# Kernel optimization log

Measured on AMD Instinct MI355X. Metric: run time of the kernel, lower is better.

The kernel has to match this reference:

```python
import jax, jax.numpy as jnp
import numpy as np

N_QUBITS = 8
BATCH = 65536
PI = float(np.pi)


def rz_mat(t):
    # diag(e^{-i t/2}, e^{+i t/2}); t scalar or [B]
    t = jnp.asarray(t, jnp.float32).astype(jnp.complex64)
    e = jnp.exp(-0.5j * t)
    z = jnp.zeros_like(e)
    return jnp.stack([jnp.stack([e, z], -1), jnp.stack([z, jnp.conj(e)], -1)], -2)


def ry_mat(t):
    t = jnp.asarray(t, jnp.float32)
    c = jnp.cos(0.5 * t).astype(jnp.complex64)
    s = jnp.sin(0.5 * t).astype(jnp.complex64)
    return jnp.stack([jnp.stack([c, -s], -1), jnp.stack([s, c], -1)], -2)


def u3_mat(t, p, l):
    t = jnp.asarray(t, jnp.float32)
    c = jnp.cos(0.5 * t).astype(jnp.complex64)
    s = jnp.sin(0.5 * t).astype(jnp.complex64)
    ep = jnp.exp(1j * jnp.asarray(p, jnp.float32).astype(jnp.complex64))
    el = jnp.exp(1j * jnp.asarray(l, jnp.float32).astype(jnp.complex64))
    return jnp.stack([jnp.stack([c, -el * s], -1), jnp.stack([ep * s, ep * el * c], -1)], -2)


def apply_1q(state, U, w):
    # state: [B] + [2]*N_QUBITS; wire w is axis w+1 (wire 0 most significant, tq convention)
    s = jnp.moveaxis(state, w + 1, -1)
    if U.ndim == 3:  # batched gate (state prep with per-sample angles)
        s = jnp.einsum('b...i,bji->b...j', s, U)
    else:
        s = jnp.einsum('...i,ji->...j', s, U)
    return jnp.moveaxis(s, -1, w + 1)


def apply_cnot(state, c, t):
    s = jnp.moveaxis(state, (c + 1, t + 1), (-2, -1))
    s = jnp.concatenate([s[..., :1, :], s[..., 1:, ::-1]], axis=-2)
    return jnp.moveaxis(s, (-2, -1), (c + 1, t + 1))


def expval_z(state, w):
    p = jnp.square(jnp.abs(state))
    p = jnp.moveaxis(p, w + 1, 1).reshape(p.shape[0], 2, -1).sum(-1)
    return p[:, 0] - p[:, 1]


def build_state(x):
    # circuit_builder substitute: RY(theta), RZ(phi) on every qubit from |0...0>
    B = x.shape[0]
    theta, phi = x[:, 0], x[:, 1]
    state = jnp.zeros((B, 2 ** N_QUBITS), jnp.complex64).at[:, 0].set(1.0)
    state = state.reshape((B,) + (2,) * N_QUBITS)
    Ry, Rz = ry_mat(theta), rz_mat(phi)  # [B,2,2]
    for w in range(N_QUBITS):
        state = apply_1q(state, Ry, w)
        state = apply_1q(state, Rz, w)
    return state


def block(state, a, b, rzp, ry1p, ry2p, fin=None):
    # ZNOTY two-qubit convolution unitary on wires (a, b)
    fin = b if fin is None else fin
    state = apply_1q(state, rz_mat(-PI / 2), a)
    state = apply_cnot(state, a, b)
    state = apply_1q(state, rz_mat(rzp), b)
    state = apply_1q(state, ry_mat(ry1p), a)
    state = apply_cnot(state, b, a)
    state = apply_1q(state, ry_mat(ry2p), a)
    state = apply_cnot(state, a, b)
    state = apply_1q(state, rz_mat(PI / 2), fin)
    return state


def qcnn_forward(x, rz_params, ry_params, u3_params, W1, b1, W2, b2):
    s = build_state(x)
    # conv layer 1 (rz2, rz5, rz8, rz11 -> indices 1,4,7,10)
    s = block(s, 1, 0, rz_params[1], ry_params[0], ry_params[1])
    s = block(s, 3, 2, rz_params[4], ry_params[2], ry_params[3])
    s = block(s, 5, 4, rz_params[7], ry_params[4], ry_params[5])
    s = block(s, 7, 6, rz_params[10], ry_params[6], ry_params[7])
    # (mid-circuit expvals on [0,2,4,6] are non-destructive and discarded -> no state change)
    for i, w in enumerate([1, 3, 5, 7]):
        s = apply_1q(s, u3_mat(u3_params[i, 0], u3_params[i, 1], u3_params[i, 2]), w)
    # conv layer 2 (rz14, rz17, rz20 -> indices 13,16,19); (7,5) block's final fixed RZ
    # lands on wire 1 (as in the original source)
    s = block(s, 3, 1, rz_params[13], ry_params[8], ry_params[9])
    s = block(s, 7, 5, rz_params[16], ry_params[10], ry_params[11], fin=1)
    s = block(s, 5, 3, rz_params[19], ry_params[12], ry_params[13])
    s = apply_1q(s, u3_mat(u3_params[4, 0], u3_params[4, 1], u3_params[4, 2]), 3)
    s = apply_1q(s, u3_mat(u3_params[5, 0], u3_params[5, 1], u3_params[5, 2]), 7)
    feats = jnp.stack([expval_z(s, 3), expval_z(s, 7)], axis=-1)  # [B,2]
    h = jnp.tanh(feats @ W1 + b1)
    return jax.nn.sigmoid(h @ W2 + b2)  # [B,1]


def setup_inputs() -> dict:
    key = jax.random.key(0)
    ks = jax.random.split(key, 8)
    return {
        'x': jax.random.normal(ks[0], (BATCH, 2), jnp.float32),
        'rz_params': jax.random.normal(ks[1], (21,), jnp.float32),
        'ry_params': jax.random.normal(ks[2], (14,), jnp.float32),
        'u3_params': jax.random.normal(ks[3], (6, 3), jnp.float32),
        'W1': jax.random.normal(ks[4], (2, 10), jnp.float32) * 0.5,
        'b1': jax.random.normal(ks[5], (10,), jnp.float32) * 0.1,
        'W2': jax.random.normal(ks[6], (10, 1), jnp.float32) * 0.5,
        'b2': jax.random.normal(ks[7], (1,), jnp.float32) * 0.1,
    }


def reference(x, rz_params, ry_params, u3_params, W1, b1, W2, b2):
    return qcnn_forward(x, rz_params, ry_params, u3_params, W1, b1, W2, b2)
```

## Files before the change

### kernel.cpp

```cpp
#include <hip/hip_runtime.h>
#include <math.h>


#define QF 0.70710678118654752f
#define GSTR 257

__device__ __forceinline__ float2 cmad2(float2 A, float2 a, float2 B, float2 b) {
  return make_float2(A.x*a.x - A.y*a.y + B.x*b.x - B.y*b.y,
                     A.x*a.y + A.y*a.x + B.x*b.y + B.y*b.x);
}

template<int CTRL>
__device__ __forceinline__ float dpps(float v) {
  int r = __builtin_amdgcn_update_dpp(__float_as_int(v), __float_as_int(v),
                                      CTRL, 0xF, 0xF, false);
  return __int_as_float(r);
}

template<int M>
__device__ __forceinline__ float lxs(float v, int lane) {
  if constexpr (M == 1)       return dpps<0xB1>(v);
  else if constexpr (M == 2)  return dpps<0x4E>(v);
  else if constexpr (M == 8)  return dpps<0x128>(v);
  else {
    int addr = (lane ^ M) << 2;
    return __int_as_float(__builtin_amdgcn_ds_bpermute(addr, __float_as_int(v)));
  }
}

template<int M>
__device__ __forceinline__ void xl8(const float2 (&z)[4], int lane,
                                    float (&px)[4], float (&py)[4]) {
#pragma unroll
  for (int j = 0; j < 4; ++j) px[j] = lxs<M>(z[j].x, lane);
#pragma unroll
  for (int j = 0; j < 4; ++j) py[j] = lxs<M>(z[j].y, lane);
}

template<int M>
__device__ __forceinline__ void rzdc(float2 (&z)[4], int lane, float c, float s) {
#pragma unroll
  for (int j = 0; j < 4; ++j) {
    bool hi;
    if constexpr (M < 64) hi = (lane & M) != 0;
    else                  hi = (j & (M >> 6)) != 0;
    float si = hi ? s : -s;
    z[j] = make_float2(c * z[j].x - si * z[j].y,
                       c * z[j].y + si * z[j].x);
  }
}

template<int M>
__device__ __forceinline__ void gate1r(float2 (&z)[4],
                                       float2 u00, float2 u01,
                                       float2 u10, float2 u11) {
  constexpr int jb = M >> 6;
#pragma unroll
  for (int j = 0; j < 4; ++j) {
    if ((j & jb) == 0) {
      float2 a = z[j], b = z[j + jb];
      z[j]      = cmad2(u00, a, u01, b);
      z[j + jb] = cmad2(u10, a, u11, b);
    }
  }
}

template<int M>
__device__ __forceinline__ void gate1c(float2 (&z)[4], int lane,
                                       float2 u00, float2 u01,
                                       float2 u10, float2 u11) {
  float px[4], py[4];
  xl8<M>(z, lane, px, py);
  bool hi = (lane & M) != 0;
  float2 A = hi ? u11 : u00;
  float2 B = hi ? u10 : u01;
#pragma unroll
  for (int j = 0; j < 4; ++j)
    z[j] = cmad2(A, z[j], B, make_float2(px[j], py[j]));
}

template<int M>
__device__ __forceinline__ void rygc(float2 (&z)[4], int lane, float c, float s) {
  if constexpr (M < 64) {
    float px[4], py[4];
    xl8<M>(z, lane, px, py);
    float sg = (lane & M) ? s : -s;
#pragma unroll
    for (int j = 0; j < 4; ++j)
      z[j] = make_float2(c * z[j].x + sg * px[j], c * z[j].y + sg * py[j]);
  } else {
    gate1r<M>(z, make_float2(c, 0.f), make_float2(-s, 0.f),
                 make_float2(s, 0.f), make_float2(c, 0.f));
  }
}

template<int M>
__device__ __forceinline__ void u3c(float2 (&z)[4], int lane,
                                    float2 u00, float2 u01,
                                    float2 u10, float2 u11) {
  if constexpr (M < 64) gate1c<M>(z, lane, u00, u01, u10, u11);
  else                  gate1r<M>(z, u00, u01, u10, u11);
}

template<int MC, int MT>
__device__ __forceinline__ void cnotg(float2 (&z)[4], int lane) {
  if constexpr (MT < 64) {
    float px[4], py[4];
#pragma unroll
    for (int j = 0; j < 4; ++j)
      if ((MC < 64) || (((j << 6) & MC) != 0)) px[j] = lxs<MT>(z[j].x, lane);
#pragma unroll
    for (int j = 0; j < 4; ++j)
      if ((MC < 64) || (((j << 6) & MC) != 0)) py[j] = lxs<MT>(z[j].y, lane);
#pragma unroll
    for (int j = 0; j < 4; ++j) {
      if ((MC < 64) || (((j << 6) & MC) != 0)) {
        bool sel = (MC >= 64) || ((lane & MC) != 0);
        z[j].x = sel ? px[j] : z[j].x;
        z[j].y = sel ? py[j] : z[j].y;
      }
    }
  } else {
    constexpr int jb = MT >> 6;
#pragma unroll
    for (int j = 0; j < 4; ++j) {
      if ((j & jb) == 0) {
        if (MC >= 64) {
          constexpr int cjb = MC >> 6;
          if ((j & cjb) != 0) { float2 t = z[j]; z[j] = z[j + jb]; z[j + jb] = t; }
        } else {
          bool sel = (lane & MC) != 0;
          float2 a = z[j], b = z[j + jb];
          z[j]      = make_float2(sel ? b.x : a.x, sel ? b.y : a.y);
          z[j + jb] = make_float2(sel ? a.x : b.x, sel ? a.y : b.y);
        }
      }
    }
  }
}

template<int MA, int MB, int MF>
__device__ __forceinline__ void blockgc(float2 (&z)[4], int lane,
                                        float2 zc, float2 y1, float2 y2) {
  rzdc<MA>(z, lane, QF, -QF);
  cnotg<MA, MB>(z, lane);
  rzdc<MB>(z, lane, zc.x, zc.y);
  rygc<MA>(z, lane, y1.x, y1.y);
  cnotg<MB, MA>(z, lane);
  rygc<MA>(z, lane, y2.x, y2.y);
  cnotg<MA, MB>(z, lane);
  rzdc<MF>(z, lane, QF, QF);
}

__device__ __forceinline__ float fast_tanh(float x) {
  float e = __expf(2.f * x);
  return 1.f - 2.f / (e + 1.f);
}

__global__ __launch_bounds__(64)
void qcnn_sim(const float* __restrict__ rz, const float* __restrict__ ry,
              const float* __restrict__ u3, float2* __restrict__ G) {
  int lane = threadIdx.x;
  int p = blockIdx.x;

  float rzl[21], ryl[14], u3l[18];
#pragma unroll
  for (int k = 0; k < 21; ++k) rzl[k] = rz[k];
#pragma unroll
  for (int k = 0; k < 14; ++k) ryl[k] = ry[k];
#pragma unroll
  for (int k = 0; k < 18; ++k) u3l[k] = u3[k];

  float2 brz[7], by1[7], by2[7];
#pragma unroll
  for (int i = 0; i < 7; ++i) {
    __sincosf(0.5f * rzl[3*i+1], &brz[i].y, &brz[i].x);
    __sincosf(0.5f * ryl[2*i],   &by1[i].y, &by1[i].x);
    __sincosf(0.5f * ryl[2*i+1], &by2[i].y, &by2[i].x);
  }
  float2 U00[6], U01[6], U10[6], U11[6];
#pragma unroll
  for (int g = 0; g < 6; ++g) {
    float s, c;   __sincosf(0.5f * u3l[3*g], &s, &c);
    float sp, cp; __sincosf(u3l[3*g+1], &sp, &cp);
    float sl, cl; __sincosf(u3l[3*g+2], &sl, &cl);
    float spl, cpl; __sincosf(u3l[3*g+1] + u3l[3*g+2], &spl, &cpl);
    U00[g] = make_float2(c, 0.f);
    U01[g] = make_float2(-cl * s, -sl * s);
    U10[g] = make_float2(cp * s, sp * s);
    U11[g] = make_float2(cpl * c, spl * c);
  }

  float2 z[4];
#pragma unroll
  for (int j = 0; j < 4; ++j) {
    int k = (j << 6) | lane;
    z[j] = make_float2(__popc(k) == p ? 1.f : 0.f, 0.f);
  }

  blockgc<1, 8, 8>(z, lane, brz[0], by1[0], by2[0]);
  blockgc<64, 4, 4>(z, lane, brz[1], by1[1], by2[1]);
  blockgc<128, 16, 16>(z, lane, brz[2], by1[2], by2[2]);
  blockgc<2, 32, 32>(z, lane, brz[3], by1[3], by2[3]);
  u3c<1>(z, lane, U00[0], U01[0], U10[0], U11[0]);
  u3c<64>(z, lane, U00[1], U01[1], U10[1], U11[1]);
  u3c<128>(z, lane, U00[2], U01[2], U10[2], U11[2]);
  u3c<2>(z, lane, U00[3], U01[3], U10[3], U11[3]);
  blockgc<64, 1, 1>(z, lane, brz[4], by1[4], by2[4]);
  blockgc<2, 128, 1>(z, lane, brz[5], by1[5], by2[5]);
  blockgc<128, 64, 64>(z, lane, brz[6], by1[6], by2[6]);
  u3c<64>(z, lane, U00[4], U01[4], U10[4], U11[4]);
  u3c<2>(z, lane, U00[5], U01[5], U10[5], U11[5]);

#pragma unroll
  for (int j = 0; j < 4; ++j)
    G[p * 256 + (j << 6) + lane] = z[j];
}

__device__ __forceinline__ void tdec(int idx, int& pp, int& qq) {
  int base = 0; pp = 0;
  while (idx >= base + 9 - pp) { base += 9 - pp; ++pp; }
  qq = pp + (idx - base);
}

__global__ __launch_bounds__(256)
void qcnn_eval(const float* __restrict__ x, const float2* __restrict__ G,
               const float* __restrict__ W1, const float* __restrict__ b1,
               const float* __restrict__ W2, const float* __restrict__ b2,
               float* __restrict__ out, int B) {
  __shared__ float2 gl[9 * GSTR];
  __shared__ float4 part[4][45];
  __shared__ float4 stab[45];
  int tid = threadIdx.x;
  int wid = tid >> 6, lane = tid & 63;

  int i = blockIdx.x * 256 + tid;
  float2 tp = reinterpret_cast<const float2*>(x)[i < B ? i : 0];

  float W1l[20], b1l[10], W2l[10], b2l;
#pragma unroll
  for (int k = 0; k < 20; ++k) W1l[k] = W1[k];
#pragma unroll
  for (int k = 0; k < 10; ++k) b1l[k] = b1[k];
#pragma unroll
  for (int k = 0; k < 10; ++k) W2l[k] = W2[k];
  b2l = b2[0];

#pragma unroll
  for (int w = 0; w < 9; ++w)
    gl[w * GSTR + tid] = G[w * 256 + tid];

  float th = tp.x, ph = tp.y;
  float stt, ct;
  __sincosf(0.5f * th, &stt, &ct);
  float c1, s1;
  __sincosf(ph, &s1, &c1);

  __syncthreads();

  if (lane < 45) {
    int pp, qq; tdec(lane, pp, qq);
    const float2* rp = &gl[pp * GSTR + (wid << 6)];
    const float2* rq = &gl[qq * GSTR + (wid << 6)];
    float pr_ = 0.f, pi_ = 0.f, mr_ = 0.f, mi_ = 0.f;
#pragma unroll
    for (int kk = 0; kk < 64; kk += 4) {
#pragma unroll
      for (int u = 0; u < 4; ++u) {
        float2 a = rp[kk + u];
        float2 b = rq[kk + u];
        float cr = a.x * b.x + a.y * b.y;
        float ci = a.x * b.y - a.y * b.x;
        if (u < 2) { pr_ += cr; pi_ += ci; }
        else       { mr_ += cr; mi_ += ci; }
      }
    }
    float s3w = (wid & 1) ? -1.f : 1.f;
    part[wid][lane] = make_float4(s3w * (pr_ + mr_), s3w * (pi_ + mi_),
                                  pr_ - mr_, pi_ - mi_);
  }
  __syncthreads();

  if (tid < 45) {
    int pp, qq; tdec(tid, pp, qq);
    float4 p0 = part[0][tid], p1 = part[1][tid];
    float4 p2 = part[2][tid], p3 = part[3][tid];
    float sc = (pp == qq) ? 1.f : 2.f;
    stab[tid] = make_float4(sc * (p0.x + p1.x + p2.x + p3.x),
                            sc * (p0.y + p1.y + p2.y + p3.y),
                            sc * (p0.z + p1.z + p2.z + p3.z),
                            sc * (p0.w + p1.w + p2.w + p3.w));
  }
  __syncthreads();

  if (i >= B) return;

  float cpw[17], spw[17];
  cpw[0] = 1.f; spw[0] = 1.f;
#pragma unroll
  for (int k = 1; k < 17; ++k) { cpw[k] = cpw[k-1] * ct; spw[k] = spw[k-1] * stt; }

  float cd[9], sd[9];
  cd[0] = 1.f; sd[0] = 0.f;
  cd[1] = c1;  sd[1] = s1;
#pragma unroll
  for (int d = 2; d < 9; ++d) {
    cd[d] = cd[d-1] * c1 - sd[d-1] * s1;
    sd[d] = sd[d-1] * c1 + cd[d-1] * s1;
  }

  float f3 = 0.f, f7 = 0.f;
  int sidx = 0;
#pragma unroll
  for (int pp = 0; pp < 9; ++pp) {
#pragma unroll
    for (int qq = pp; qq < 9; ++qq) {
      float4 s4 = stab[sidx]; ++sidx;
      float w = cpw[16 - pp - qq] * spw[pp + qq];
      int d = qq - pp;
      f3 += w * (s4.x * cd[d] - s4.y * sd[d]);
      f7 += w * (s4.z * cd[d] - s4.w * sd[d]);
    }
  }

  float acc = b2l;
#pragma unroll
  for (int j = 0; j < 10; ++j) {
    float h = fast_tanh(f3 * W1l[j] + f7 * W1l[10 + j] + b1l[j]);
    acc += h * W2l[j];
  }
  out[i] = 1.f / (1.f + __expf(-acc));
}

extern "C" void kernel_launch(void* const* d_in, const int* in_sizes, int n_in,
                              void* d_out, int out_size, void* d_ws, size_t ws_size,
                              hipStream_t stream) {
  const float* x  = (const float*)d_in[0];
  const float* rz = (const float*)d_in[1];
  const float* ry = (const float*)d_in[2];
  const float* u3 = (const float*)d_in[3];
  const float* W1 = (const float*)d_in[4];
  const float* b1 = (const float*)d_in[5];
  const float* W2 = (const float*)d_in[6];
  const float* b2 = (const float*)d_in[7];

  float2* G = (float2*)d_ws;

  qcnn_sim<<<9, 64, 0, stream>>>(rz, ry, u3, G);

  int B = in_sizes[0] / 2;
  qcnn_eval<<<(B + 255) / 256, 256, 0, stream>>>(x, G, W1, b1, W2, b2,
                                                 (float*)d_out, B);
}
```

Baseline: 16.52 us.

## Fuse circuit simulation into eval kernel, recomputing basis states per block

Merges the 9-block simulation kernel into the evaluation kernel. Each 576-thread block runs the nine 64-lane circuit simulations itself, writes them straight to shared memory and then evaluates 512 samples. This removes a kernel launch, the global round trip through the workspace and the dependency between the two kernels. The cost is redundant simulation in every block (128 blocks instead of 9) and larger blocks with higher register pressure.

```diff
diff --git a/kernel.cpp b/kernel.cpp
--- a/kernel.cpp
+++ b/kernel.cpp
@@ -157,11 +157,36 @@
   return 1.f - 2.f / (e + 1.f);
 }
 
-__global__ __launch_bounds__(64)
-void qcnn_sim(const float* __restrict__ rz, const float* __restrict__ ry,
-              const float* __restrict__ u3, float2* __restrict__ G) {
-  int lane = threadIdx.x;
-  int p = blockIdx.x;
+__device__ __forceinline__ void tdec(int idx, int& pp, int& qq) {
+  int base = 0; pp = 0;
+  while (idx >= base + 9 - pp) { base += 9 - pp; ++pp; }
+  qq = pp + (idx - base);
+}
+
+__global__ __launch_bounds__(576)
+void qcnn_fused(const float* __restrict__ x, const float* __restrict__ rz,
+                const float* __restrict__ ry, const float* __restrict__ u3,
+                const float* __restrict__ W1, const float* __restrict__ b1,
+                const float* __restrict__ W2, const float* __restrict__ b2,
+                float* __restrict__ out, int B) {
+  __shared__ float2 gl[9 * GSTR];
+  __shared__ float4 part[4][45];
+  __shared__ float4 stab[45];
+  int tid = threadIdx.x;
+  int p = tid >> 6, lane = tid & 63;
+
+  int i = blockIdx.x * 512 + tid;
+  float2 tp = make_float2(0.f, 0.f);
+  if (tid < 512) tp = reinterpret_cast<const float2*>(x)[i < B ? i : 0];
+
+  float W1l[20], b1l[10], W2l[10], b2l;
+#pragma unroll
+  for (int k = 0; k < 20; ++k) W1l[k] = W1[k];
+#pragma unroll
+  for (int k = 0; k < 10; ++k) b1l[k] = b1[k];
+#pragma unroll
+  for (int k = 0; k < 10; ++k) W2l[k] = W2[k];
+  b2l = b2[0];
 
   float rzl[21], ryl[14], u3l[18];
 #pragma unroll
@@ -173,10 +198,10 @@
 
   float2 brz[7], by1[7], by2[7];
 #pragma unroll
-  for (int i = 0; i < 7; ++i) {
-    __sincosf(0.5f * rzl[3*i+1], &brz[i].y, &brz[i].x);
-    __sincosf(0.5f * ryl[2*i],   &by1[i].y, &by1[i].x);
-    __sincosf(0.5f * ryl[2*i+1], &by2[i].y, &by2[i].x);
+  for (int v = 0; v < 7; ++v) {
+    __sincosf(0.5f * rzl[3*v+1], &brz[v].y, &brz[v].x);
+    __sincosf(0.5f * ryl[2*v],   &by1[v].y, &by1[v].x);
+    __sincosf(0.5f * ryl[2*v+1], &by2[v].y, &by2[v].x);
   }
   float2 U00[6], U01[6], U10[6], U11[6];
 #pragma unroll
@@ -214,41 +239,7 @@
 
 #pragma unroll
   for (int j = 0; j < 4; ++j)
-    G[p * 256 + (j << 6) + lane] = z[j];
-}
-
-__device__ __forceinline__ void tdec(int idx, int& pp, int& qq) {
-  int base = 0; pp = 0;
-  while (idx >= base + 9 - pp) { base += 9 - pp; ++pp; }
-  qq = pp + (idx - base);
-}
-
-__global__ __launch_bounds__(256)
-void qcnn_eval(const float* __restrict__ x, const float2* __restrict__ G,
-               const float* __restrict__ W1, const float* __restrict__ b1,
-               const float* __restrict__ W2, const float* __restrict__ b2,
-               float* __restrict__ out, int B) {
-  __shared__ float2 gl[9 * GSTR];
-  __shared__ float4 part[4][45];
-  __shared__ float4 stab[45];
-  int tid = threadIdx.x;
-  int wid = tid >> 6, lane = tid & 63;
-
-  int i = blockIdx.x * 256 + tid;
-  float2 tp = reinterpret_cast<const float2*>(x)[i < B ? i : 0];
-
-  float W1l[20], b1l[10], W2l[10], b2l;
-#pragma unroll
-  for (int k = 0; k < 20; ++k) W1l[k] = W1[k];
-#pragma unroll
-  for (int k = 0; k < 10; ++k) b1l[k] = b1[k];
-#pragma unroll
-  for (int k = 0; k < 10; ++k) W2l[k] = W2[k];
-  b2l = b2[0];
-
-#pragma unroll
-  for (int w = 0; w < 9; ++w)
-    gl[w * GSTR + tid] = G[w * 256 + tid];
+    gl[p * GSTR + (j << 6) + lane] = z[j];
 
   float th = tp.x, ph = tp.y;
   float stt, ct;
@@ -258,10 +249,10 @@
 
   __syncthreads();
 
-  if (lane < 45) {
+  if (p < 4 && lane < 45) {
     int pp, qq; tdec(lane, pp, qq);
-    const float2* rp = &gl[pp * GSTR + (wid << 6)];
-    const float2* rq = &gl[qq * GSTR + (wid << 6)];
+    const float2* rp = &gl[pp * GSTR + (p << 6)];
+    const float2* rq = &gl[qq * GSTR + (p << 6)];
     float pr_ = 0.f, pi_ = 0.f, mr_ = 0.f, mi_ = 0.f;
 #pragma unroll
     for (int kk = 0; kk < 64; kk += 4) {
@@ -275,9 +266,9 @@
         else       { mr_ += cr; mi_ += ci; }
       }
     }
-    float s3w = (wid & 1) ? -1.f : 1.f;
-    part[wid][lane] = make_float4(s3w * (pr_ + mr_), s3w * (pi_ + mi_),
-                                  pr_ - mr_, pi_ - mi_);
+    float s3w = (p & 1) ? -1.f : 1.f;
+    part[p][lane] = make_float4(s3w * (pr_ + mr_), s3w * (pi_ + mi_),
+                                pr_ - mr_, pi_ - mi_);
   }
   __syncthreads();
 
@@ -293,7 +284,7 @@
   }
   __syncthreads();
 
-  if (i >= B) return;
+  if (tid >= 512 || i >= B) return;
 
   float cpw[17], spw[17];
   cpw[0] = 1.f; spw[0] = 1.f;
@@ -344,11 +335,8 @@
   const float* W2 = (const float*)d_in[6];
   const float* b2 = (const float*)d_in[7];
 
-  float2* G = (float2*)d_ws;
-
-  qcnn_sim<<<9, 64, 0, stream>>>(rz, ry, u3, G);
-
   int B = in_sizes[0] / 2;
-  qcnn_eval<<<(B + 255) / 256, 256, 0, stream>>>(x, G, W1, b1, W2, b2,
-                                                 (float*)d_out, B);
-}
+  int grid = (B + 511) / 512;
+  qcnn_fused<<<grid, 576, 0, stream>>>(x, rz, ry, u3, W1, b1, W2, b2,
+                                       (float*)d_out, B);
+}
```

New measurement: 20.72 us. 1.25x slower.
